# Performance work log

Measured on AMD Instinct MI355X. Metric: run time of the kernel, lower is better.

Reference implementation:

```python
import jax, jax.numpy as jnp
import numpy as np

B, S, H, U = 32, 4096, 512, 512


def setup_inputs() -> dict:
    key = jax.random.key(0)
    ks = jax.random.split(key, 6)
    scale = 1.0 / np.sqrt(H)
    return {
        "query": jax.random.normal(ks[0], (B, H), dtype=jnp.float32),
        "values": jax.random.normal(ks[1], (B, S, H), dtype=jnp.float32),
        "W1": jax.random.normal(ks[2], (H, U), dtype=jnp.float32) * scale,
        "b1": jnp.zeros((U,), dtype=jnp.float32),
        "W2": jax.random.normal(ks[3], (H, U), dtype=jnp.float32) * scale,
        "b2": jnp.zeros((U,), dtype=jnp.float32),
        "va": jax.random.normal(ks[4], (U, 1), dtype=jnp.float32) * (1.0 / np.sqrt(U)),
        "bva": jnp.zeros((1,), dtype=jnp.float32),
    }


def reference(query, values, W1, b1, W2, b2, va, bva):
    # query: [B, H] -> [B, 1, U]; values: [B, S, H] -> [B, S, U]
    q_proj = jnp.einsum('bh,hu->bu', query, W1) + b1           # [B, U]
    v_proj = jnp.einsum('bsh,hu->bsu', values, W2) + b2        # [B, S, U]
    scores = jnp.einsum('bsu,uo->bso', jnp.tanh(q_proj[:, None, :] + v_proj), va) + bva  # [B, S, 1]
    attention_weights = jax.nn.softmax(scores, axis=1)         # [B, S, 1]
    context_vector = jnp.sum(attention_weights * values, axis=1)  # [B, H]
    return attention_weights, context_vector
```

## Files before the change

### kernel.cpp

```cpp
#include <hip/hip_runtime.h>
#include <hip/hip_bf16.h>
#include <stdint.h>

#define B_SZ 32
#define S_SZ 4096
#define H_SZ 512
#define U_SZ 512

typedef __attribute__((ext_vector_type(8))) _Float16 half8;
typedef __attribute__((ext_vector_type(4))) float floatx4;

__device__ __forceinline__ void async_copy16(const void* g, void* l) {
    __builtin_amdgcn_global_load_lds(
        (const __attribute__((address_space(1))) void*)g,
        (__attribute__((address_space(3))) void*)l, 16, 0, 0);
}

__global__ __launch_bounds__(256) void prep_kernel(
    const float* __restrict__ values, const float* __restrict__ W2,
    const float* __restrict__ b1, const float* __restrict__ b2,
    const float* __restrict__ bva, const float* __restrict__ query,
    const float* __restrict__ W1, _Float16* __restrict__ W2s,
    float* __restrict__ qpb2, float* __restrict__ scores,
    float* __restrict__ ctx, _Float16* __restrict__ vf16, int nconv)
{
    const int t = threadIdx.x;
    const int bid = blockIdx.x;
    if (bid < nconv) {
        const size_t i = ((size_t)bid * 256 + t) * 8;
        float4 v0 = *(const float4*)(values + i);
        float4 v1 = *(const float4*)(values + i + 4);
        half8 h;
        h[0] = (_Float16)v0.x; h[1] = (_Float16)v0.y;
        h[2] = (_Float16)v0.z; h[3] = (_Float16)v0.w;
        h[4] = (_Float16)v1.x; h[5] = (_Float16)v1.y;
        h[6] = (_Float16)v1.z; h[7] = (_Float16)v1.w;
        *(half8*)(vf16 + i) = h;
        return;
    }
    const int rb = bid - nconv;
    if (rb < 1024) {
        const int i = rb * 256 + t;
        const int k = i >> 9, n = i & 511;
        W2s[(k >> 5) * 16384 + ((k >> 3) & 3) * 4096 + n * 8 + (k & 7)] =
            (_Float16)W2[i];
    } else if (rb < 1536) {
        scores[(rb - 1024) * 256 + t] = *bva;
    } else if (rb < 1600) {
        ctx[(rb - 1536) * 256 + t] = 0.0f;
    } else {
        const int bq = rb - 1600;
        const int b = bq >> 1, uc = bq & 1;
        const int u = uc * 256 + t;
        const float* q  = query + b * H_SZ;
        const float* Wp = W1 + u;
        float a0 = 0.f, a1 = 0.f, a2 = 0.f, a3 = 0.f;
        for (int k = 0; k < 512; k += 4) {
            a0 = fmaf(q[k],     Wp[(size_t)k * U_SZ],       a0);
            a1 = fmaf(q[k + 1], Wp[(size_t)(k + 1) * U_SZ], a1);
            a2 = fmaf(q[k + 2], Wp[(size_t)(k + 2) * U_SZ], a2);
            a3 = fmaf(q[k + 3], Wp[(size_t)(k + 3) * U_SZ], a3);
        }
        qpb2[b * U_SZ + u] = (a0 + a1) + (a2 + a3) + b1[u] + b2[u];
    }
}

template <typename AT>
__global__ __launch_bounds__(256, 4) void scores_kernel(
    const AT* __restrict__ A, const _Float16* __restrict__ W2s,
    const float* __restrict__ qpb2, const float* __restrict__ va,
    float* __restrict__ scores)
{
    __shared__ __align__(16) AT       Albs[2][4096];
    __shared__ __align__(16) _Float16 Blbs[2][4096];
    __shared__ float red[256];

    const int t  = threadIdx.x;
    const int w  = t >> 6, l = t & 63;
    const int c  = l & 15, g4 = l >> 4;
    const int mh = w >> 1, nh = w & 1;
    const int n0 = (blockIdx.x & 3) * 128;
    const int m0 = (blockIdx.x >> 2) * 128;
    const int b  = m0 >> 12;

    floatx4 acc[4][4];
#pragma unroll
    for (int mt = 0; mt < 4; ++mt)
#pragma unroll
        for (int nt = 0; nt < 4; ++nt) acc[mt][nt] = (floatx4)(0.0f);

    const AT*       Ab0 = A + (size_t)m0 * H_SZ;
    const _Float16* Wb0 = W2s + n0 * 8;

    auto stage = [&](int kb, int buf) {
        const AT* Vb = Ab0 + kb * 32;
        if constexpr (sizeof(AT) == 4) {
#pragma unroll
            for (int i = 0; i < 4; ++i) {
                const int j = t + i * 256;
                const int g = j >> 7, ml = j & 127;
                async_copy16(Vb + (size_t)ml * H_SZ + g * 4, &Albs[buf][j * 4]);
            }
        } else {
#pragma unroll
            for (int i = 0; i < 2; ++i) {
                const int j = t + i * 256;
                const int g = j >> 7, ml = j & 127;
                async_copy16(Vb + (size_t)ml * H_SZ + g * 8, &Albs[buf][j * 8]);
            }
        }
        const _Float16* Wb = Wb0 + kb * 16384;
#pragma unroll
        for (int i = 0; i < 2; ++i) {
            const int j = t + i * 256;
            const int kq = j >> 7, nl = j & 127;
            async_copy16(Wb + kq * 4096 + nl * 8, &Blbs[buf][j * 8]);
        }
    };

    stage(0, 0);
    __syncthreads();

    for (int kb = 0; kb < 16; ++kb) {
        const int cur = kb & 1;
        if (kb < 15) stage(kb + 1, cur ^ 1);
        half8 af[4];
#pragma unroll
        for (int mt = 0; mt < 4; ++mt) {
            const int ml = mh * 64 + mt * 16 + c;
            if constexpr (sizeof(AT) == 4) {
                float4 lo = *(const float4*)&Albs[cur][((2 * g4)     * 128 + ml) * 4];
                float4 hi = *(const float4*)&Albs[cur][((2 * g4 + 1) * 128 + ml) * 4];
                half8 a;
                a[0] = (_Float16)lo.x; a[1] = (_Float16)lo.y;
                a[2] = (_Float16)lo.z; a[3] = (_Float16)lo.w;
                a[4] = (_Float16)hi.x; a[5] = (_Float16)hi.y;
                a[6] = (_Float16)hi.z; a[7] = (_Float16)hi.w;
                af[mt] = a;
            } else {
                af[mt] = *(const half8*)&Albs[cur][(g4 * 128 + ml) * 8];
            }
        }
        half8 bf[4];
#pragma unroll
        for (int nt = 0; nt < 4; ++nt) {
            const int nl = nh * 64 + nt * 16 + c;
            bf[nt] = *(const half8*)&Blbs[cur][(g4 * 128 + nl) * 8];
        }
#pragma unroll
        for (int mt = 0; mt < 4; ++mt)
#pragma unroll
            for (int nt = 0; nt < 4; ++nt)
                acc[mt][nt] = __builtin_amdgcn_mfma_f32_16x16x32_f16(
                    af[mt], bf[nt], acc[mt][nt], 0, 0, 0);
        __syncthreads();
    }

    float qv2[4], vv[4], vv2[4];
#pragma unroll
    for (int nt = 0; nt < 4; ++nt) {
        const int n = n0 + nh * 64 + nt * 16 + c;
        const float q = qpb2[b * U_SZ + n];
        const float v = va[n];
        qv2[nt] = 2.0f * q;
        vv[nt] = v;
        vv2[nt] = 2.0f * v;
    }
#pragma unroll
    for (int mt = 0; mt < 4; ++mt) {
#pragma unroll
        for (int r = 0; r < 4; ++r) {
            float p = 0.0f;
#pragma unroll
            for (int nt = 0; nt < 4; ++nt) {
                const float ex = __expf(fmaf(acc[mt][nt][r], 2.0f, qv2[nt]));
                const float rc = __builtin_amdgcn_rcpf(ex + 1.0f);
                p = fmaf(-vv2[nt], rc, p + vv[nt]);
            }
            p += __shfl_xor(p, 1);
            p += __shfl_xor(p, 2);
            p += __shfl_xor(p, 4);
            p += __shfl_xor(p, 8);
            if (c == 0)
                red[(mh * 64 + mt * 16 + g4 * 4 + r) * 2 + nh] = p;
        }
    }
    __syncthreads();
    if (t < 128)
        atomicAdd(&scores[m0 + t], red[t * 2] + red[t * 2 + 1]);
}

__global__ __launch_bounds__(1024) void sredux_kernel(
    const float* __restrict__ scores, float* __restrict__ ML)
{
    __shared__ float red[16];
    __shared__ float s_max;
    const int b = blockIdx.x;
    const int t = threadIdx.x;
    float4 v = *(const float4*)(scores + b * S_SZ + t * 4);
    float m = fmaxf(fmaxf(v.x, v.y), fmaxf(v.z, v.w));
#pragma unroll
    for (int o = 32; o > 0; o >>= 1) m = fmaxf(m, __shfl_xor(m, o));
    if ((t & 63) == 0) red[t >> 6] = m;
    __syncthreads();
    if (t == 0) {
        float mm = red[0];
        for (int i = 1; i < 16; ++i) mm = fmaxf(mm, red[i]);
        s_max = mm;
    }
    __syncthreads();
    const float mm = s_max;
    float s = __expf(v.x - mm) + __expf(v.y - mm) +
              __expf(v.z - mm) + __expf(v.w - mm);
#pragma unroll
    for (int o = 32; o > 0; o >>= 1) s += __shfl_xor(s, o);
    if ((t & 63) == 0) red[t >> 6] = s;
    __syncthreads();
    if (t == 0) {
        float ss = 0.0f;
        for (int i = 0; i < 16; ++i) ss += red[i];
        ML[b * 2] = mm;
        ML[b * 2 + 1] = ss;
    }
}

__global__ __launch_bounds__(256) void context_f16_kernel(
    const _Float16* __restrict__ vf16, const float* __restrict__ scores,
    const float* __restrict__ ML, float* __restrict__ out)
{
    __shared__ float wl[128];
    __shared__ float part[4][512];
    const int sc = blockIdx.x, b = blockIdx.y;
    const int t = threadIdx.x;
    const int s0 = sc * 128;
    const float M = ML[b * 2];
    const float rL = 1.0f / ML[b * 2 + 1];
    if (t < 32) {
        float4 sv = *(const float4*)(scores + b * S_SZ + s0 + t * 4);
        float4 wv;
        wv.x = __expf(sv.x - M) * rL; wv.y = __expf(sv.y - M) * rL;
        wv.z = __expf(sv.z - M) * rL; wv.w = __expf(sv.w - M) * rL;
        *(float4*)&wl[t * 4] = wv;
        *(float4*)(out + b * S_SZ + s0 + t * 4) = wv;
    }
    __syncthreads();

    const int g = t >> 6, l = t & 63;
    const _Float16* vp = vf16 + ((size_t)b * S_SZ + s0 + g * 32) * H_SZ + l * 8;
    float a[4][8];
#pragma unroll
    for (int u = 0; u < 4; ++u)
#pragma unroll
        for (int e = 0; e < 8; ++e) a[u][e] = 0.0f;
    for (int i = 0; i < 32; i += 4) {
#pragma unroll
        for (int u = 0; u < 4; ++u) {
            const float wu = wl[g * 32 + i + u];
            half8 hv = *(const half8*)(vp + (size_t)(i + u) * H_SZ);
#pragma unroll
            for (int e = 0; e < 8; ++e)
                a[u][e] = fmaf(wu, (float)hv[e], a[u][e]);
        }
    }
#pragma unroll
    for (int e = 0; e < 8; ++e)
        part[g][l * 8 + e] = (a[0][e] + a[1][e]) + (a[2][e] + a[3][e]);
    __syncthreads();

    float* ctx = out + B_SZ * S_SZ;
#pragma unroll
    for (int rep = 0; rep < 2; ++rep) {
        const int h = rep * 256 + t;
        const float s = (part[0][h] + part[1][h]) + (part[2][h] + part[3][h]);
        atomicAdd(&ctx[b * H_SZ + h], s);
    }
}

__global__ __launch_bounds__(256) void context_f32_kernel(
    const float* __restrict__ values, const float* __restrict__ scores,
    const float* __restrict__ ML, float* __restrict__ out)
{
    __shared__ float wl[128];
    __shared__ __align__(16) float part[4][512];
    const int sc = blockIdx.x, b = blockIdx.y;
    const int t = threadIdx.x;
    const int s0 = sc * 128;
    const float M = ML[b * 2];
    const float rL = 1.0f / ML[b * 2 + 1];
    if (t < 32) {
        float4 sv = *(const float4*)(scores + b * S_SZ + s0 + t * 4);
        float4 wv;
        wv.x = __expf(sv.x - M) * rL; wv.y = __expf(sv.y - M) * rL;
        wv.z = __expf(sv.z - M) * rL; wv.w = __expf(sv.w - M) * rL;
        *(float4*)&wl[t * 4] = wv;
        *(float4*)(out + b * S_SZ + s0 + t * 4) = wv;
    }
    __syncthreads();

    const int g = t >> 6, l = t & 63;
    const float* vp = values + ((size_t)b * S_SZ + s0 + g * 32) * H_SZ + l * 4;
    float4 a00 = {0,0,0,0}, a01 = {0,0,0,0}, a10 = {0,0,0,0}, a11 = {0,0,0,0};
    for (int i = 0; i < 32; i += 2) {
        const float w0 = wl[g * 32 + i];
        const float w1 = wl[g * 32 + i + 1];
        const float* r0 = vp + (size_t)i * H_SZ;
        const float* r1 = r0 + H_SZ;
        float4 v00 = *(const float4*)(r0);
        float4 v01 = *(const float4*)(r0 + 256);
        float4 v10 = *(const float4*)(r1);
        float4 v11 = *(const float4*)(r1 + 256);
        a00.x = fmaf(w0, v00.x, a00.x); a00.y = fmaf(w0, v00.y, a00.y);
        a00.z = fmaf(w0, v00.z, a00.z); a00.w = fmaf(w0, v00.w, a00.w);
        a01.x = fmaf(w0, v01.x, a01.x); a01.y = fmaf(w0, v01.y, a01.y);
        a01.z = fmaf(w0, v01.z, a01.z); a01.w = fmaf(w0, v01.w, a01.w);
        a10.x = fmaf(w1, v10.x, a10.x); a10.y = fmaf(w1, v10.y, a10.y);
        a10.z = fmaf(w1, v10.z, a10.z); a10.w = fmaf(w1, v10.w, a10.w);
        a11.x = fmaf(w1, v11.x, a11.x); a11.y = fmaf(w1, v11.y, a11.y);
        a11.z = fmaf(w1, v11.z, a11.z); a11.w = fmaf(w1, v11.w, a11.w);
    }
    a00.x += a10.x; a00.y += a10.y; a00.z += a10.z; a00.w += a10.w;
    a01.x += a11.x; a01.y += a11.y; a01.z += a11.z; a01.w += a11.w;
    *(float4*)&part[g][l * 4] = a00;
    *(float4*)&part[g][256 + l * 4] = a01;
    __syncthreads();

    float* ctx = out + B_SZ * S_SZ;
#pragma unroll
    for (int rep = 0; rep < 2; ++rep) {
        const int h = rep * 256 + t;
        const float s = (part[0][h] + part[1][h]) + (part[2][h] + part[3][h]);
        atomicAdd(&ctx[b * H_SZ + h], s);
    }
}

extern "C" void kernel_launch(void* const* d_in, const int* in_sizes, int n_in,
                              void* d_out, int out_size, void* d_ws, size_t ws_size,
                              hipStream_t stream) {
    const float* query  = (const float*)d_in[0];
    const float* values = (const float*)d_in[1];
    const float* W1     = (const float*)d_in[2];
    const float* b1     = (const float*)d_in[3];
    const float* W2     = (const float*)d_in[4];
    const float* b2     = (const float*)d_in[5];
    const float* va     = (const float*)d_in[6];
    const float* bva    = (const float*)d_in[7];
    float* out = (float*)d_out;

    char* ws = (char*)d_ws;
    float*    qpb2   = (float*)ws;
    _Float16* W2s    = (_Float16*)(ws + 65536);
    float*    scores = (float*)(ws + 589824);
    float*    ML     = (float*)(ws + 1114112);
    _Float16* vf16   = (_Float16*)(ws + 1118208);

    const size_t NEED = 1118208ull + 134217728ull;
    const bool f16path = ws_size >= NEED;
    const int nconv = f16path ? 32768 : 0;

    float* ctx = out + B_SZ * S_SZ;

    prep_kernel<<<nconv + 1664, 256, 0, stream>>>(
        values, W2, b1, b2, bva, query, W1, W2s, qpb2, scores, ctx, vf16, nconv);
    if (f16path) {
        scores_kernel<_Float16><<<4096, 256, 0, stream>>>(vf16, W2s, qpb2, va, scores);
    } else {
        scores_kernel<float><<<4096, 256, 0, stream>>>(values, W2s, qpb2, va, scores);
    }
    sredux_kernel<<<32, 1024, 0, stream>>>(scores, ML);
    if (f16path) {
        context_f16_kernel<<<dim3(32, 32), 256, 0, stream>>>(vf16, scores, ML, out);
    } else {
        context_f32_kernel<<<dim3(32, 32), 256, 0, stream>>>(values, scores, ML, out);
    }
}
```

Before: 542.8 us.

## Drop f16 pre-conversion of values and remap scores block order across XCDs

Removes the separate pass that converts the whole values tensor to fp16 in workspace, and instead always reads fp32 values directly in the scores GEMM (converting in registers) and in the fp32 context kernel. This eliminates a full extra read plus half-size write and re-read of the 256MB values tensor. The scores kernel also remaps block indices so consecutive blocks on each XCD share the same M tile across the four N tiles, improving L2 reuse of the values rows. The trade-off is double the bytes per GEMM tile load and per context read compared with the f16 copy.

```diff
diff --git a/kernel.cpp b/kernel.cpp
--- a/kernel.cpp
+++ b/kernel.cpp
@@ -1,5 +1,4 @@
 #include <hip/hip_runtime.h>
-#include <hip/hip_bf16.h>
 #include <stdint.h>
 
 #define B_SZ 32
@@ -17,28 +16,14 @@
 }
 
 __global__ __launch_bounds__(256) void prep_kernel(
-    const float* __restrict__ values, const float* __restrict__ W2,
-    const float* __restrict__ b1, const float* __restrict__ b2,
-    const float* __restrict__ bva, const float* __restrict__ query,
-    const float* __restrict__ W1, _Float16* __restrict__ W2s,
-    float* __restrict__ qpb2, float* __restrict__ scores,
-    float* __restrict__ ctx, _Float16* __restrict__ vf16, int nconv)
+    const float* __restrict__ W2, const float* __restrict__ b1,
+    const float* __restrict__ b2, const float* __restrict__ bva,
+    const float* __restrict__ query, const float* __restrict__ W1,
+    _Float16* __restrict__ W2s, float* __restrict__ qpb2,
+    float* __restrict__ scores, float* __restrict__ ctx)
 {
     const int t = threadIdx.x;
-    const int bid = blockIdx.x;
-    if (bid < nconv) {
-        const size_t i = ((size_t)bid * 256 + t) * 8;
-        float4 v0 = *(const float4*)(values + i);
-        float4 v1 = *(const float4*)(values + i + 4);
-        half8 h;
-        h[0] = (_Float16)v0.x; h[1] = (_Float16)v0.y;
-        h[2] = (_Float16)v0.z; h[3] = (_Float16)v0.w;
-        h[4] = (_Float16)v1.x; h[5] = (_Float16)v1.y;
-        h[6] = (_Float16)v1.z; h[7] = (_Float16)v1.w;
-        *(half8*)(vf16 + i) = h;
-        return;
-    }
-    const int rb = bid - nconv;
+    const int rb = blockIdx.x;
     if (rb < 1024) {
         const int i = rb * 256 + t;
         const int k = i >> 9, n = i & 511;
@@ -65,13 +50,12 @@
     }
 }
 
-template <typename AT>
 __global__ __launch_bounds__(256, 4) void scores_kernel(
-    const AT* __restrict__ A, const _Float16* __restrict__ W2s,
+    const float* __restrict__ A, const _Float16* __restrict__ W2s,
     const float* __restrict__ qpb2, const float* __restrict__ va,
     float* __restrict__ scores)
 {
-    __shared__ __align__(16) AT       Albs[2][4096];
+    __shared__ __align__(16) float    Albs[2][4096];
     __shared__ __align__(16) _Float16 Blbs[2][4096];
     __shared__ float red[256];
 
@@ -79,8 +63,10 @@
     const int w  = t >> 6, l = t & 63;
     const int c  = l & 15, g4 = l >> 4;
     const int mh = w >> 1, nh = w & 1;
-    const int n0 = (blockIdx.x & 3) * 128;
-    const int m0 = (blockIdx.x >> 2) * 128;
+    const int bidx = (int)blockIdx.x;
+    const int lb   = (bidx & 7) * 512 + (bidx >> 3);
+    const int n0 = (lb & 3) * 128;
+    const int m0 = (lb >> 2) * 128;
     const int b  = m0 >> 12;
 
     floatx4 acc[4][4];
@@ -89,25 +75,16 @@
 #pragma unroll
         for (int nt = 0; nt < 4; ++nt) acc[mt][nt] = (floatx4)(0.0f);
 
-    const AT*       Ab0 = A + (size_t)m0 * H_SZ;
+    const float*    Ab0 = A + (size_t)m0 * H_SZ;
     const _Float16* Wb0 = W2s + n0 * 8;
 
     auto stage = [&](int kb, int buf) {
-        const AT* Vb = Ab0 + kb * 32;
-        if constexpr (sizeof(AT) == 4) {
-#pragma unroll
-            for (int i = 0; i < 4; ++i) {
-                const int j = t + i * 256;
-                const int g = j >> 7, ml = j & 127;
-                async_copy16(Vb + (size_t)ml * H_SZ + g * 4, &Albs[buf][j * 4]);
-            }
-        } else {
-#pragma unroll
-            for (int i = 0; i < 2; ++i) {
-                const int j = t + i * 256;
-                const int g = j >> 7, ml = j & 127;
-                async_copy16(Vb + (size_t)ml * H_SZ + g * 8, &Albs[buf][j * 8]);
-            }
+        const float* Vb = Ab0 + kb * 32;
+#pragma unroll
+        for (int i = 0; i < 4; ++i) {
+            const int j = t + i * 256;
+            const int g = j >> 7, ml = j & 127;
+            async_copy16(Vb + (size_t)ml * H_SZ + g * 4, &Albs[buf][j * 4]);
         }
         const _Float16* Wb = Wb0 + kb * 16384;
 #pragma unroll
@@ -128,18 +105,14 @@
 #pragma unroll
         for (int mt = 0; mt < 4; ++mt) {
             const int ml = mh * 64 + mt * 16 + c;
-            if constexpr (sizeof(AT) == 4) {
-                float4 lo = *(const float4*)&Albs[cur][((2 * g4)     * 128 + ml) * 4];
-                float4 hi = *(const float4*)&Albs[cur][((2 * g4 + 1) * 128 + ml) * 4];
-                half8 a;
-                a[0] = (_Float16)lo.x; a[1] = (_Float16)lo.y;
-                a[2] = (_Float16)lo.z; a[3] = (_Float16)lo.w;
-                a[4] = (_Float16)hi.x; a[5] = (_Float16)hi.y;
-                a[6] = (_Float16)hi.z; a[7] = (_Float16)hi.w;
-                af[mt] = a;
-            } else {
-                af[mt] = *(const half8*)&Albs[cur][(g4 * 128 + ml) * 8];
-            }
+            float4 lo = *(const float4*)&Albs[cur][((2 * g4)     * 128 + ml) * 4];
+            float4 hi = *(const float4*)&Albs[cur][((2 * g4 + 1) * 128 + ml) * 4];
+            half8 a;
+            a[0] = (_Float16)lo.x; a[1] = (_Float16)lo.y;
+            a[2] = (_Float16)lo.z; a[3] = (_Float16)lo.w;
+            a[4] = (_Float16)hi.x; a[5] = (_Float16)hi.y;
+            a[6] = (_Float16)hi.z; a[7] = (_Float16)hi.w;
+            af[mt] = a;
         }
         half8 bf[4];
 #pragma unroll
@@ -221,58 +194,6 @@
         for (int i = 0; i < 16; ++i) ss += red[i];
         ML[b * 2] = mm;
         ML[b * 2 + 1] = ss;
-    }
-}
-
-__global__ __launch_bounds__(256) void context_f16_kernel(
-    const _Float16* __restrict__ vf16, const float* __restrict__ scores,
-    const float* __restrict__ ML, float* __restrict__ out)
-{
-    __shared__ float wl[128];
-    __shared__ float part[4][512];
-    const int sc = blockIdx.x, b = blockIdx.y;
-    const int t = threadIdx.x;
-    const int s0 = sc * 128;
-    const float M = ML[b * 2];
-    const float rL = 1.0f / ML[b * 2 + 1];
-    if (t < 32) {
-        float4 sv = *(const float4*)(scores + b * S_SZ + s0 + t * 4);
-        float4 wv;
-        wv.x = __expf(sv.x - M) * rL; wv.y = __expf(sv.y - M) * rL;
-        wv.z = __expf(sv.z - M) * rL; wv.w = __expf(sv.w - M) * rL;
-        *(float4*)&wl[t * 4] = wv;
-        *(float4*)(out + b * S_SZ + s0 + t * 4) = wv;
-    }
-    __syncthreads();
-
-    const int g = t >> 6, l = t & 63;
-    const _Float16* vp = vf16 + ((size_t)b * S_SZ + s0 + g * 32) * H_SZ + l * 8;
-    float a[4][8];
-#pragma unroll
-    for (int u = 0; u < 4; ++u)
-#pragma unroll
-        for (int e = 0; e < 8; ++e) a[u][e] = 0.0f;
-    for (int i = 0; i < 32; i += 4) {
-#pragma unroll
-        for (int u = 0; u < 4; ++u) {
-            const float wu = wl[g * 32 + i + u];
-            half8 hv = *(const half8*)(vp + (size_t)(i + u) * H_SZ);
-#pragma unroll
-            for (int e = 0; e < 8; ++e)
-                a[u][e] = fmaf(wu, (float)hv[e], a[u][e]);
-        }
-    }
-#pragma unroll
-    for (int e = 0; e < 8; ++e)
-        part[g][l * 8 + e] = (a[0][e] + a[1][e]) + (a[2][e] + a[3][e]);
-    __syncthreads();
-
-    float* ctx = out + B_SZ * S_SZ;
-#pragma unroll
-    for (int rep = 0; rep < 2; ++rep) {
-        const int h = rep * 256 + t;
-        const float s = (part[0][h] + part[1][h]) + (part[2][h] + part[3][h]);
-        atomicAdd(&ctx[b * H_SZ + h], s);
     }
 }
 
@@ -351,25 +272,12 @@
     _Float16* W2s    = (_Float16*)(ws + 65536);
     float*    scores = (float*)(ws + 589824);
     float*    ML     = (float*)(ws + 1114112);
-    _Float16* vf16   = (_Float16*)(ws + 1118208);
-
-    const size_t NEED = 1118208ull + 134217728ull;
-    const bool f16path = ws_size >= NEED;
-    const int nconv = f16path ? 32768 : 0;
 
     float* ctx = out + B_SZ * S_SZ;
 
-    prep_kernel<<<nconv + 1664, 256, 0, stream>>>(
-        values, W2, b1, b2, bva, query, W1, W2s, qpb2, scores, ctx, vf16, nconv);
-    if (f16path) {
-        scores_kernel<_Float16><<<4096, 256, 0, stream>>>(vf16, W2s, qpb2, va, scores);
-    } else {
-        scores_kernel<float><<<4096, 256, 0, stream>>>(values, W2s, qpb2, va, scores);
-    }
+    prep_kernel<<<1664, 256, 0, stream>>>(
+        W2, b1, b2, bva, query, W1, W2s, qpb2, scores, ctx);
+    scores_kernel<<<4096, 256, 0, stream>>>(values, W2s, qpb2, va, scores);
     sredux_kernel<<<32, 1024, 0, stream>>>(scores, ML);
-    if (f16path) {
-        context_f16_kernel<<<dim3(32, 32), 256, 0, stream>>>(vf16, scores, ML, out);
-    } else {
-        context_f32_kernel<<<dim3(32, 32), 256, 0, stream>>>(values, scores, ML, out);
-    }
-}
+    context_f32_kernel<<<dim3(32, 32), 256, 0, stream>>>(values, scores, ML, out);
+}
```

Result: slower. 586.1 us (+8.0%).
